# Kernel optimization log

Hardware: AMD Instinct MI355X
Metric: run time of the kernel (lower is better)

The kernel has to match this reference:

```python
import jax, jax.numpy as jnp
import numpy as np

B, LQ, LK, D, H = 4, 1024, 1024, 512, 8
HD = D // H
NEG_SLOPE = 0.2


def setup_inputs() -> dict:
    key = jax.random.key(0)
    k1, k2, k3, k4, k5 = jax.random.split(key, 5)
    query = jax.random.normal(k1, (B, LQ, D), dtype=jnp.float32)
    key_t = jax.random.normal(k2, (B, LK, D), dtype=jnp.float32)
    value = jax.random.normal(k3, (B, LK, D), dtype=jnp.float32)
    mask = jnp.ones((B, LQ, LK), dtype=jnp.int32)
    # xavier-uniform-like init for params
    limW = float(np.sqrt(6.0 / (D + D)))
    W = jax.random.uniform(k4, (D, D), minval=-limW, maxval=limW, dtype=jnp.float32)
    lima = float(np.sqrt(6.0 / (H + 2 * HD)))
    a = jax.random.uniform(k5, (1, H, 2 * HD), minval=-lima, maxval=lima, dtype=jnp.float32)
    return {"query": query, "key": key_t, "value": value, "mask": mask, "W": W, "a": a}


def reference(query, key, value, mask, W, a):
    b, lq, d = query.shape
    lk = key.shape[1]
    h = a.shape[1]
    hd = a.shape[2] // 2
    # shared linear projection (nn.Linear: x @ W.T)
    Q = (query @ W.T).reshape(b, lq, h, hd)
    K = (key @ W.T).reshape(b, lk, h, hd)
    V = (value @ W.T).reshape(b, lk, h, hd)
    # a^T [Q || K] = a_q . Q + a_k . K  (avoids the (b,lq,lk,h,2hd) concat)
    a_q = a[0, :, :hd]  # (h, hd)
    a_k = a[0, :, hd:]
    sq = jnp.einsum('bqhd,hd->bhq', Q, a_q)
    sk = jnp.einsum('bkhd,hd->bhk', K, a_k)
    scores = sq[:, :, :, None] + sk[:, :, None, :]  # (b, h, lq, lk)
    scores = jnp.where(scores >= 0, scores, NEG_SLOPE * scores)  # LeakyReLU
    scores = jnp.where(mask[:, None, :, :] == 0, -jnp.inf, scores)
    attn = jax.nn.softmax(scores, axis=-1)
    attn = jnp.where(jnp.isnan(attn), 0.0, attn)  # fully-masked rows -> 0
    out = jnp.einsum('bhqk,bkhd->bqhd', attn, V).reshape(b, lq, d)
    return out
```

## Files before the change

kernel.cpp:

```cpp
#include <hip/hip_runtime.h>
#include <hip/hip_bf16.h>

#define NEG_SLOPE 0.2f

constexpr int B = 4, LQ = 1024, LK = 1024, D = 512, H = 8, HD = 64;

typedef __attribute__((ext_vector_type(8))) short bf16x8;
typedef __attribute__((ext_vector_type(4))) float f32x4;

static __device__ __forceinline__ ushort f2bf(float x) {
  return __builtin_bit_cast(ushort, __float2bfloat16(x));
}
static __device__ __forceinline__ float bf2f(ushort u) {
  return __bfloat162float(__builtin_bit_cast(__hip_bfloat16, u));
}

__global__ void prep_wqwk(const float* __restrict__ W, const float* __restrict__ a,
                          float* __restrict__ wq, float* __restrict__ wk) {
  int tid = blockIdx.x * blockDim.x + threadIdx.x;
  int h = tid >> 9, j = tid & 511;
  const float* aq = a + h * 2 * HD;
  const float* ak = aq + HD;
  float accq = 0.f, acck = 0.f;
#pragma unroll 8
  for (int d = 0; d < HD; ++d) {
    float w = W[(size_t)(h * HD + d) * D + j];
    accq = fmaf(aq[d], w, accq);
    acck = fmaf(ak[d], w, acck);
  }
  wq[tid] = accq;
  wk[tid] = acck;
}

__global__ __launch_bounds__(256) void sqsk_kernel(
    const float* __restrict__ query, const float* __restrict__ key,
    const float* __restrict__ wq, const float* __restrict__ wk,
    float* __restrict__ sq, float* __restrict__ sk) {
  int gw = (blockIdx.x * blockDim.x + threadIdx.x) >> 6;
  int lane = threadIdx.x & 63;
  bool isK = gw >= B * LQ;
  int row = isK ? gw - B * LQ : gw;
  const float* x = (isK ? key : query) + (size_t)row * D + lane * 8;
  const float* wbase = isK ? wk : wq;
  float4 x0 = *(const float4*)x;
  float4 x1 = *(const float4*)(x + 4);
  float acc[H];
#pragma unroll
  for (int h = 0; h < H; ++h) {
    const float* w = wbase + h * D + lane * 8;
    float4 w0 = *(const float4*)w;
    float4 w1 = *(const float4*)(w + 4);
    acc[h] = x0.x * w0.x + x0.y * w0.y + x0.z * w0.z + x0.w * w0.w +
             x1.x * w1.x + x1.y * w1.y + x1.z * w1.z + x1.w * w1.w;
  }
#pragma unroll
  for (int off = 32; off > 0; off >>= 1) {
#pragma unroll
    for (int h = 0; h < H; ++h) acc[h] += __shfl_xor(acc[h], off, 64);
  }
  if (lane == 0) {
    int b = row >> 10, pos = row & 1023;
    float* dst = isK ? sk : sq;
#pragma unroll
    for (int h = 0; h < H; ++h) dst[((size_t)(b * H + h) << 10) + pos] = acc[h];
  }
}

__global__ __launch_bounds__(256) void cvt_split(
    const float* __restrict__ value, const float* __restrict__ W,
    ushort* __restrict__ val_hi, ushort* __restrict__ val_lo,
    ushort* __restrict__ w_hi, ushort* __restrict__ w_lo) {
  constexpr int VAL4 = B * LK * D / 4;
  constexpr int W4 = D * D / 4;
  int idx = blockIdx.x * 256 + threadIdx.x;
  if (idx >= VAL4 + W4) return;
  const float* src;
  ushort *dhi, *dlo;
  int off;
  if (idx < VAL4) { src = value; dhi = val_hi; dlo = val_lo; off = idx; }
  else           { src = W;     dhi = w_hi;   dlo = w_lo;   off = idx - VAL4; }
  float4 x = ((const float4*)src)[off];
  float xs[4] = {x.x, x.y, x.z, x.w};
  ushort hs[4], ls[4];
#pragma unroll
  for (int i = 0; i < 4; ++i) {
    hs[i] = f2bf(xs[i]);
    ls[i] = f2bf(xs[i] - bf2f(hs[i]));
  }
  ((ushort4*)dhi)[off] = make_ushort4(hs[0], hs[1], hs[2], hs[3]);
  ((ushort4*)dlo)[off] = make_ushort4(ls[0], ls[1], ls[2], ls[3]);
}

__global__ __launch_bounds__(256) void maskbits_kernel(const int* __restrict__ mask,
                                                       unsigned int* __restrict__ mbits) {
  int gw = (blockIdx.x * 256 + threadIdx.x) >> 6;
  int lane = threadIdx.x & 63;
#pragma unroll 4
  for (int it = 0; it < 64; ++it) {
    int wv = gw + it * 1024;
    int mv = mask[(size_t)wv * 64 + lane];
    unsigned long long bal = __ballot(mv != 0);
    if (lane == 0) *(unsigned long long*)&mbits[wv * 2] = bal;
  }
}

__global__ __launch_bounds__(256) void vproj_mfma(
    const ushort* __restrict__ val_hi, const ushort* __restrict__ val_lo,
    const ushort* __restrict__ w_hi, const ushort* __restrict__ w_lo,
    ushort* __restrict__ vt_hi, ushort* __restrict__ vt_lo) {
  __shared__ ushort as_hi[64][40], as_lo[64][40], bs_hi[64][40], bs_lo[64][40];
  int r0 = blockIdx.x * 64, c0 = blockIdx.y * 64;
  int tid = threadIdx.x, w = tid >> 6, lane = tid & 63;
  int wr = w >> 1, wc = w & 1;
  int ln15 = lane & 15, kg = lane >> 4;
  f32x4 acc[2][2] = {};
  int srow = tid >> 2, sch = (tid & 3) * 8;
  for (int k0 = 0; k0 < D; k0 += 32) {
    __syncthreads();
    *(float4*)&as_hi[srow][sch] = *(const float4*)&val_hi[(size_t)(r0 + srow) * D + k0 + sch];
    *(float4*)&as_lo[srow][sch] = *(const float4*)&val_lo[(size_t)(r0 + srow) * D + k0 + sch];
    *(float4*)&bs_hi[srow][sch] = *(const float4*)&w_hi[(size_t)(c0 + srow) * D + k0 + sch];
    *(float4*)&bs_lo[srow][sch] = *(const float4*)&w_lo[(size_t)(c0 + srow) * D + k0 + sch];
    __syncthreads();
    bf16x8 ah[2], al[2], bh[2], bl[2];
#pragma unroll
    for (int f = 0; f < 2; ++f) {
      int ra = wr * 32 + f * 16 + ln15;
      ah[f] = *(const bf16x8*)&as_hi[ra][kg * 8];
      al[f] = *(const bf16x8*)&as_lo[ra][kg * 8];
      int rb = wc * 32 + f * 16 + ln15;
      bh[f] = *(const bf16x8*)&bs_hi[rb][kg * 8];
      bl[f] = *(const bf16x8*)&bs_lo[rb][kg * 8];
    }
#pragma unroll
    for (int fm = 0; fm < 2; ++fm)
#pragma unroll
      for (int fn = 0; fn < 2; ++fn) {
        acc[fm][fn] = __builtin_amdgcn_mfma_f32_16x16x32_bf16(ah[fm], bh[fn], acc[fm][fn], 0, 0, 0);
        acc[fm][fn] = __builtin_amdgcn_mfma_f32_16x16x32_bf16(al[fm], bh[fn], acc[fm][fn], 0, 0, 0);
        acc[fm][fn] = __builtin_amdgcn_mfma_f32_16x16x32_bf16(ah[fm], bl[fn], acc[fm][fn], 0, 0, 0);
      }
  }
#pragma unroll
  for (int fm = 0; fm < 2; ++fm)
#pragma unroll
    for (int fn = 0; fn < 2; ++fn) {
      int rrow = r0 + wr * 32 + fm * 16 + (lane >> 4) * 4;
      int col = c0 + wc * 32 + fn * 16 + ln15;
      int b = rrow >> 10, k = rrow & 1023;
      int h = col >> 6, dd = col & 63;
      size_t base = ((size_t)((b * H + h) * HD + dd) << 10) + k;
      ushort hv[4], lv[4];
#pragma unroll
      for (int r = 0; r < 4; ++r) {
        float v = acc[fm][fn][r];
        hv[r] = f2bf(v);
        lv[r] = f2bf(v - bf2f(hv[r]));
      }
      *(ushort4*)&vt_hi[base] = make_ushort4(hv[0], hv[1], hv[2], hv[3]);
      *(ushort4*)&vt_lo[base] = make_ushort4(lv[0], lv[1], lv[2], lv[3]);
    }
}

__global__ __launch_bounds__(256) void attn_mfma(
    const float* __restrict__ sq, const float* __restrict__ sk,
    const unsigned int* __restrict__ mbits,
    const ushort* __restrict__ vt_hi, const ushort* __restrict__ vt_lo,
    float* __restrict__ out) {
  __shared__ float sks[LK];
  __shared__ ushort vhs[64][136], vls[64][136];
  __shared__ float linv_s[4][16];
  int bh = blockIdx.x, b = bh >> 3, h = bh & 7;
  int q0 = blockIdx.y * 64;
  int tid = threadIdx.x, w = tid >> 6, lane = tid & 63;
  int ln15 = lane & 15, kg = lane >> 4;
  int qs = q0 + w * 16 + ln15;
#pragma unroll
  for (int i = 0; i < 4; ++i) sks[i * 256 + tid] = sk[((size_t)bh << 10) + i * 256 + tid];
  float sqv = sq[((size_t)bh << 10) + qs];
  const unsigned int* mrow = mbits + ((size_t)(b << 10) + qs) * (LK / 32);
  const ushort* vhbase = vt_hi + (((size_t)bh * HD) << 10);
  const ushort* vlbase = vt_lo + (((size_t)bh * HD) << 10);
  f32x4 acc[4] = {};
  float lsum = 0.f;
  for (int tile = 0; tile < 8; ++tile) {
    int k0 = tile * 128;
    __syncthreads();
#pragma unroll
    for (int c = 0; c < 4; ++c) {
      int id = c * 256 + tid;
      int d = id >> 4, ch = id & 15;
      *(float4*)&vhs[d][ch * 8] = *(const float4*)&vhbase[((size_t)d << 10) + k0 + ch * 8];
      *(float4*)&vls[d][ch * 8] = *(const float4*)&vlbase[((size_t)d << 10) + k0 + ch * 8];
    }
    __syncthreads();
#pragma unroll
    for (int ks = 0; ks < 4; ++ks) {
      int kb = k0 + ks * 32;
      unsigned int wb = mrow[kb >> 5];
      float skv[8];
      *(float4*)&skv[0] = *(const float4*)&sks[kb + kg * 8];
      *(float4*)&skv[4] = *(const float4*)&sks[kb + kg * 8 + 4];
      bf16x8 phi, plo;
#pragma unroll
      for (int i = 0; i < 8; ++i) {
        float s = sqv + skv[i];
        float f = fmaxf(s, NEG_SLOPE * s);
        float p = ((wb >> (kg * 8 + i)) & 1u) ? __expf(f - 8.0f) : 0.f;
        lsum += p;
        ushort hb = f2bf(p);
        phi[i] = (short)hb;
        plo[i] = (short)f2bf(p - bf2f(hb));
      }
#pragma unroll
      for (int df = 0; df < 4; ++df) {
        int drow = df * 16 + ln15;
        bf16x8 bhv = *(const bf16x8*)&vhs[drow][ks * 32 + kg * 8];
        bf16x8 blv = *(const bf16x8*)&vls[drow][ks * 32 + kg * 8];
        acc[df] = __builtin_amdgcn_mfma_f32_16x16x32_bf16(phi, bhv, acc[df], 0, 0, 0);
        acc[df] = __builtin_amdgcn_mfma_f32_16x16x32_bf16(plo, bhv, acc[df], 0, 0, 0);
        acc[df] = __builtin_amdgcn_mfma_f32_16x16x32_bf16(phi, blv, acc[df], 0, 0, 0);
      }
    }
  }
  lsum += __shfl_xor(lsum, 16, 64);
  lsum += __shfl_xor(lsum, 32, 64);
  if (lane < 16) linv_s[w][ln15] = (lsum > 0.f) ? 1.f / lsum : 0.f;
  __syncthreads();
#pragma unroll
  for (int df = 0; df < 4; ++df) {
#pragma unroll
    for (int r = 0; r < 4; ++r) {
      int qrow = q0 + w * 16 + (lane >> 4) * 4 + r;
      float inv = linv_s[w][(lane >> 4) * 4 + r];
      int col = h * HD + df * 16 + ln15;
      out[((size_t)(b << 10) + qrow) * D + col] = acc[df][r] * inv;
    }
  }
}

extern "C" void kernel_launch(void* const* d_in, const int* in_sizes, int n_in,
                              void* d_out, int out_size, void* d_ws, size_t ws_size,
                              hipStream_t stream) {
  const float* query = (const float*)d_in[0];
  const float* key   = (const float*)d_in[1];
  const float* value = (const float*)d_in[2];
  const int*   mask  = (const int*)d_in[3];
  const float* W     = (const float*)d_in[4];
  const float* a     = (const float*)d_in[5];
  float* out = (float*)d_out;

  char* ws = (char*)d_ws;
  float* wq = (float*)ws;                    ws += 4096 * 4;
  float* wk = (float*)ws;                    ws += 4096 * 4;
  float* sq = (float*)ws;                    ws += 32768 * 4;
  float* sk = (float*)ws;                    ws += 32768 * 4;
  ushort* val_hi = (ushort*)ws;              ws += (size_t)B * LK * D * 2;
  ushort* val_lo = (ushort*)ws;              ws += (size_t)B * LK * D * 2;
  ushort* w_hi = (ushort*)ws;                ws += (size_t)D * D * 2;
  ushort* w_lo = (ushort*)ws;                ws += (size_t)D * D * 2;
  ushort* vt_hi = (ushort*)ws;               ws += (size_t)B * H * HD * LK * 2;
  ushort* vt_lo = (ushort*)ws;               ws += (size_t)B * H * HD * LK * 2;
  unsigned int* mbits = (unsigned int*)ws;   ws += (size_t)B * LQ * LK / 32 * 4;

  prep_wqwk<<<dim3(16), dim3(256), 0, stream>>>(W, a, wq, wk);
  cvt_split<<<dim3((B * LK * D / 4 + D * D / 4 + 255) / 256), dim3(256), 0, stream>>>(
      value, W, val_hi, val_lo, w_hi, w_lo);
  maskbits_kernel<<<dim3(256), dim3(256), 0, stream>>>(mask, mbits);
  sqsk_kernel<<<dim3(2 * B * LQ / 4), dim3(256), 0, stream>>>(query, key, wq, wk, sq, sk);
  vproj_mfma<<<dim3(B * LK / 64, D / 64), dim3(256), 0, stream>>>(
      val_hi, val_lo, w_hi, w_lo, vt_hi, vt_lo);
  attn_mfma<<<dim3(B * H, LQ / 64), dim3(256), 0, stream>>>(
      sq, sk, mbits, vt_hi, vt_lo, out);
}
```

Measured before the change: 156.3 us.

## Fuse auxiliary prep kernels and restructure projection and attention with split-K reduction

Merges the bf16 split conversion, mask bit-packing and score-vector kernels into one launch, cutting per-kernel launch and tail overhead. The V projection now loads operands directly from global memory with a 4-way split-K across waves and reduces partial sums through shared memory. The attention kernel uses 32-query tiles with a 2-way split over keys, a block order chosen so that blocks landing on the same XCD share a (batch, head), and direct global loads of V instead of LDS staging. The aim is more blocks and better occupancy, in exchange for extra shared-memory reductions and uncoalesced, unshared global loads.

```diff
diff --git a/kernel.cpp b/kernel.cpp
--- a/kernel.cpp
+++ b/kernel.cpp
@@ -32,75 +32,73 @@
   wk[tid] = acck;
 }
 
-__global__ __launch_bounds__(256) void sqsk_kernel(
+__global__ __launch_bounds__(256) void fused_aux(
     const float* __restrict__ query, const float* __restrict__ key,
+    const float* __restrict__ value, const int* __restrict__ mask,
+    const float* __restrict__ W,
     const float* __restrict__ wq, const float* __restrict__ wk,
+    ushort* __restrict__ val_hi, ushort* __restrict__ val_lo,
+    ushort* __restrict__ w_hi, ushort* __restrict__ w_lo,
+    unsigned int* __restrict__ mbits,
     float* __restrict__ sq, float* __restrict__ sk) {
-  int gw = (blockIdx.x * blockDim.x + threadIdx.x) >> 6;
-  int lane = threadIdx.x & 63;
-  bool isK = gw >= B * LQ;
-  int row = isK ? gw - B * LQ : gw;
-  const float* x = (isK ? key : query) + (size_t)row * D + lane * 8;
-  const float* wbase = isK ? wk : wq;
-  float4 x0 = *(const float4*)x;
-  float4 x1 = *(const float4*)(x + 4);
-  float acc[H];
-#pragma unroll
-  for (int h = 0; h < H; ++h) {
-    const float* w = wbase + h * D + lane * 8;
-    float4 w0 = *(const float4*)w;
-    float4 w1 = *(const float4*)(w + 4);
-    acc[h] = x0.x * w0.x + x0.y * w0.y + x0.z * w0.z + x0.w * w0.w +
-             x1.x * w1.x + x1.y * w1.y + x1.z * w1.z + x1.w * w1.w;
-  }
-#pragma unroll
-  for (int off = 32; off > 0; off >>= 1) {
-#pragma unroll
-    for (int h = 0; h < H; ++h) acc[h] += __shfl_xor(acc[h], off, 64);
-  }
-  if (lane == 0) {
-    int b = row >> 10, pos = row & 1023;
-    float* dst = isK ? sk : sq;
-#pragma unroll
-    for (int h = 0; h < H; ++h) dst[((size_t)(b * H + h) << 10) + pos] = acc[h];
-  }
-}
-
-__global__ __launch_bounds__(256) void cvt_split(
-    const float* __restrict__ value, const float* __restrict__ W,
-    ushort* __restrict__ val_hi, ushort* __restrict__ val_lo,
-    ushort* __restrict__ w_hi, ushort* __restrict__ w_lo) {
-  constexpr int VAL4 = B * LK * D / 4;
-  constexpr int W4 = D * D / 4;
-  int idx = blockIdx.x * 256 + threadIdx.x;
-  if (idx >= VAL4 + W4) return;
-  const float* src;
-  ushort *dhi, *dlo;
-  int off;
-  if (idx < VAL4) { src = value; dhi = val_hi; dlo = val_lo; off = idx; }
-  else           { src = W;     dhi = w_hi;   dlo = w_lo;   off = idx - VAL4; }
-  float4 x = ((const float4*)src)[off];
-  float xs[4] = {x.x, x.y, x.z, x.w};
-  ushort hs[4], ls[4];
-#pragma unroll
-  for (int i = 0; i < 4; ++i) {
-    hs[i] = f2bf(xs[i]);
-    ls[i] = f2bf(xs[i] - bf2f(hs[i]));
-  }
-  ((ushort4*)dhi)[off] = make_ushort4(hs[0], hs[1], hs[2], hs[3]);
-  ((ushort4*)dlo)[off] = make_ushort4(ls[0], ls[1], ls[2], ls[3]);
-}
-
-__global__ __launch_bounds__(256) void maskbits_kernel(const int* __restrict__ mask,
-                                                       unsigned int* __restrict__ mbits) {
-  int gw = (blockIdx.x * 256 + threadIdx.x) >> 6;
-  int lane = threadIdx.x & 63;
-#pragma unroll 4
-  for (int it = 0; it < 64; ++it) {
-    int wv = gw + it * 1024;
-    int mv = mask[(size_t)wv * 64 + lane];
-    unsigned long long bal = __ballot(mv != 0);
-    if (lane == 0) *(unsigned long long*)&mbits[wv * 2] = bal;
+  int blk = blockIdx.x, tid = threadIdx.x;
+  if (blk < 2304) {
+    constexpr int VAL4 = B * LK * D / 4;
+    int idx = blk * 256 + tid;
+    const float* src;
+    ushort *dhi, *dlo;
+    int off;
+    if (idx < VAL4) { src = value; dhi = val_hi; dlo = val_lo; off = idx; }
+    else           { src = W;     dhi = w_hi;   dlo = w_lo;   off = idx - VAL4; }
+    float4 x = ((const float4*)src)[off];
+    float xs[4] = {x.x, x.y, x.z, x.w};
+    ushort hs[4], ls[4];
+#pragma unroll
+    for (int i = 0; i < 4; ++i) {
+      hs[i] = f2bf(xs[i]);
+      ls[i] = f2bf(xs[i] - bf2f(hs[i]));
+    }
+    ((ushort4*)dhi)[off] = make_ushort4(hs[0], hs[1], hs[2], hs[3]);
+    ((ushort4*)dlo)[off] = make_ushort4(ls[0], ls[1], ls[2], ls[3]);
+  } else if (blk < 4352) {
+    int gw = ((blk - 2304) * 256 + tid) >> 6;
+    int lane = tid & 63;
+#pragma unroll
+    for (int it = 0; it < 8; ++it) {
+      int wv = gw * 8 + it;
+      int mv = mask[(size_t)wv * 64 + lane];
+      unsigned long long bal = __ballot(mv != 0);
+      if (lane == 0) *(unsigned long long*)&mbits[wv * 2] = bal;
+    }
+  } else {
+    int gw = ((blk - 4352) * 256 + tid) >> 6;
+    int lane = tid & 63;
+    bool isK = gw >= B * LQ;
+    int row = isK ? gw - B * LQ : gw;
+    const float* x = (isK ? key : query) + (size_t)row * D + lane * 8;
+    const float* wbase = isK ? wk : wq;
+    float4 x0 = *(const float4*)x;
+    float4 x1 = *(const float4*)(x + 4);
+    float acc[H];
+#pragma unroll
+    for (int h = 0; h < H; ++h) {
+      const float* w = wbase + h * D + lane * 8;
+      float4 w0 = *(const float4*)w;
+      float4 w1 = *(const float4*)(w + 4);
+      acc[h] = x0.x * w0.x + x0.y * w0.y + x0.z * w0.z + x0.w * w0.w +
+               x1.x * w1.x + x1.y * w1.y + x1.z * w1.z + x1.w * w1.w;
+    }
+#pragma unroll
+    for (int off = 32; off > 0; off >>= 1) {
+#pragma unroll
+      for (int h = 0; h < H; ++h) acc[h] += __shfl_xor(acc[h], off, 64);
+    }
+    if (lane == 0) {
+      int b = row >> 10, pos = row & 1023;
+      float* dst = isK ? sk : sq;
+#pragma unroll
+      for (int h = 0; h < H; ++h) dst[((size_t)(b * H + h) << 10) + pos] = acc[h];
+    }
   }
 }
 
@@ -108,32 +106,28 @@
     const ushort* __restrict__ val_hi, const ushort* __restrict__ val_lo,
     const ushort* __restrict__ w_hi, const ushort* __restrict__ w_lo,
     ushort* __restrict__ vt_hi, ushort* __restrict__ vt_lo) {
-  __shared__ ushort as_hi[64][40], as_lo[64][40], bs_hi[64][40], bs_lo[64][40];
-  int r0 = blockIdx.x * 64, c0 = blockIdx.y * 64;
+  __shared__ float vred[3][64][36];
+  int c0 = blockIdx.x * 32, r0 = blockIdx.y * 64;
   int tid = threadIdx.x, w = tid >> 6, lane = tid & 63;
-  int wr = w >> 1, wc = w & 1;
   int ln15 = lane & 15, kg = lane >> 4;
-  f32x4 acc[2][2] = {};
-  int srow = tid >> 2, sch = (tid & 3) * 8;
-  for (int k0 = 0; k0 < D; k0 += 32) {
-    __syncthreads();
-    *(float4*)&as_hi[srow][sch] = *(const float4*)&val_hi[(size_t)(r0 + srow) * D + k0 + sch];
-    *(float4*)&as_lo[srow][sch] = *(const float4*)&val_lo[(size_t)(r0 + srow) * D + k0 + sch];
-    *(float4*)&bs_hi[srow][sch] = *(const float4*)&w_hi[(size_t)(c0 + srow) * D + k0 + sch];
-    *(float4*)&bs_lo[srow][sch] = *(const float4*)&w_lo[(size_t)(c0 + srow) * D + k0 + sch];
-    __syncthreads();
-    bf16x8 ah[2], al[2], bh[2], bl[2];
-#pragma unroll
-    for (int f = 0; f < 2; ++f) {
-      int ra = wr * 32 + f * 16 + ln15;
-      ah[f] = *(const bf16x8*)&as_hi[ra][kg * 8];
-      al[f] = *(const bf16x8*)&as_lo[ra][kg * 8];
-      int rb = wc * 32 + f * 16 + ln15;
-      bh[f] = *(const bf16x8*)&bs_hi[rb][kg * 8];
-      bl[f] = *(const bf16x8*)&bs_lo[rb][kg * 8];
-    }
-#pragma unroll
-    for (int fm = 0; fm < 2; ++fm)
+  f32x4 acc[4][2] = {};
+  for (int step = 0; step < 4; ++step) {
+    int kq = w * 128 + step * 32 + kg * 8;
+    bf16x8 ah[4], al[4], bh[2], bl[2];
+#pragma unroll
+    for (int fm = 0; fm < 4; ++fm) {
+      size_t off = (size_t)(r0 + fm * 16 + ln15) * D + kq;
+      ah[fm] = *(const bf16x8*)&val_hi[off];
+      al[fm] = *(const bf16x8*)&val_lo[off];
+    }
+#pragma unroll
+    for (int fn = 0; fn < 2; ++fn) {
+      size_t off = (size_t)(c0 + fn * 16 + ln15) * D + kq;
+      bh[fn] = *(const bf16x8*)&w_hi[off];
+      bl[fn] = *(const bf16x8*)&w_lo[off];
+    }
+#pragma unroll
+    for (int fm = 0; fm < 4; ++fm)
 #pragma unroll
       for (int fn = 0; fn < 2; ++fn) {
         acc[fm][fn] = __builtin_amdgcn_mfma_f32_16x16x32_bf16(ah[fm], bh[fn], acc[fm][fn], 0, 0, 0);
@@ -141,25 +135,38 @@
         acc[fm][fn] = __builtin_amdgcn_mfma_f32_16x16x32_bf16(ah[fm], bl[fn], acc[fm][fn], 0, 0, 0);
       }
   }
-#pragma unroll
-  for (int fm = 0; fm < 2; ++fm)
-#pragma unroll
-    for (int fn = 0; fn < 2; ++fn) {
-      int rrow = r0 + wr * 32 + fm * 16 + (lane >> 4) * 4;
-      int col = c0 + wc * 32 + fn * 16 + ln15;
-      int b = rrow >> 10, k = rrow & 1023;
-      int h = col >> 6, dd = col & 63;
-      size_t base = ((size_t)((b * H + h) * HD + dd) << 10) + k;
-      ushort hv[4], lv[4];
-#pragma unroll
-      for (int r = 0; r < 4; ++r) {
-        float v = acc[fm][fn][r];
-        hv[r] = f2bf(v);
-        lv[r] = f2bf(v - bf2f(hv[r]));
-      }
-      *(ushort4*)&vt_hi[base] = make_ushort4(hv[0], hv[1], hv[2], hv[3]);
-      *(ushort4*)&vt_lo[base] = make_ushort4(lv[0], lv[1], lv[2], lv[3]);
-    }
+  if (w > 0) {
+#pragma unroll
+    for (int fm = 0; fm < 4; ++fm)
+#pragma unroll
+      for (int fn = 0; fn < 2; ++fn)
+        *(f32x4*)&vred[w - 1][lane][(fm * 2 + fn) * 4] = acc[fm][fn];
+  }
+  __syncthreads();
+  if (w == 0) {
+#pragma unroll
+    for (int fm = 0; fm < 4; ++fm)
+#pragma unroll
+      for (int fn = 0; fn < 2; ++fn) {
+#pragma unroll
+        for (int k = 0; k < 3; ++k)
+          acc[fm][fn] += *(const f32x4*)&vred[k][lane][(fm * 2 + fn) * 4];
+        int rrow = r0 + fm * 16 + (lane >> 4) * 4;
+        int col = c0 + fn * 16 + ln15;
+        int bb = rrow >> 10, kk = rrow & 1023;
+        int hh = col >> 6, dd = col & 63;
+        size_t base = ((size_t)((bb * H + hh) * HD + dd) << 10) + kk;
+        ushort hv[4], lv[4];
+#pragma unroll
+        for (int r = 0; r < 4; ++r) {
+          float v = acc[fm][fn][r];
+          hv[r] = f2bf(v);
+          lv[r] = f2bf(v - bf2f(hv[r]));
+        }
+        *(ushort4*)&vt_hi[base] = make_ushort4(hv[0], hv[1], hv[2], hv[3]);
+        *(ushort4*)&vt_lo[base] = make_ushort4(lv[0], lv[1], lv[2], lv[3]);
+      }
+  }
 }
 
 __global__ __launch_bounds__(256) void attn_mfma(
@@ -168,36 +175,40 @@
     const ushort* __restrict__ vt_hi, const ushort* __restrict__ vt_lo,
     float* __restrict__ out) {
   __shared__ float sks[LK];
-  __shared__ ushort vhs[64][136], vls[64][136];
-  __shared__ float linv_s[4][16];
-  int bh = blockIdx.x, b = bh >> 3, h = bh & 7;
-  int q0 = blockIdx.y * 64;
+  __shared__ float ared[2][64][36];
+  __shared__ float lred[2][16];
+  __shared__ float linv_s[2][16];
+  int bid = blockIdx.x;
+  int xcd = bid & 7, slot = bid >> 3;
+  int bh = xcd * 4 + (slot & 3), qt = slot >> 2;
+  int b = bh >> 3, h = bh & 7;
+  int q0 = qt * 32;
   int tid = threadIdx.x, w = tid >> 6, lane = tid & 63;
+  int strip = w & 1, khalf = w >> 1;
   int ln15 = lane & 15, kg = lane >> 4;
-  int qs = q0 + w * 16 + ln15;
+  int qs = q0 + strip * 16 + ln15;
 #pragma unroll
   for (int i = 0; i < 4; ++i) sks[i * 256 + tid] = sk[((size_t)bh << 10) + i * 256 + tid];
   float sqv = sq[((size_t)bh << 10) + qs];
   const unsigned int* mrow = mbits + ((size_t)(b << 10) + qs) * (LK / 32);
   const ushort* vhbase = vt_hi + (((size_t)bh * HD) << 10);
   const ushort* vlbase = vt_lo + (((size_t)bh * HD) << 10);
+  __syncthreads();
   f32x4 acc[4] = {};
   float lsum = 0.f;
-  for (int tile = 0; tile < 8; ++tile) {
-    int k0 = tile * 128;
-    __syncthreads();
-#pragma unroll
-    for (int c = 0; c < 4; ++c) {
-      int id = c * 256 + tid;
-      int d = id >> 4, ch = id & 15;
-      *(float4*)&vhs[d][ch * 8] = *(const float4*)&vhbase[((size_t)d << 10) + k0 + ch * 8];
-      *(float4*)&vls[d][ch * 8] = *(const float4*)&vlbase[((size_t)d << 10) + k0 + ch * 8];
-    }
-    __syncthreads();
+  for (int tile = 0; tile < 4; ++tile) {
+    int kt0 = khalf * 512 + tile * 128;
 #pragma unroll
     for (int ks = 0; ks < 4; ++ks) {
-      int kb = k0 + ks * 32;
+      int kb = kt0 + ks * 32;
       unsigned int wb = mrow[kb >> 5];
+      bf16x8 bhv[4], blv[4];
+#pragma unroll
+      for (int df = 0; df < 4; ++df) {
+        size_t off = ((size_t)(df * 16 + ln15) << 10) + kb + kg * 8;
+        bhv[df] = *(const bf16x8*)&vhbase[off];
+        blv[df] = *(const bf16x8*)&vlbase[off];
+      }
       float skv[8];
       *(float4*)&skv[0] = *(const float4*)&sks[kb + kg * 8];
       *(float4*)&skv[4] = *(const float4*)&sks[kb + kg * 8 + 4];
@@ -214,27 +225,37 @@
       }
 #pragma unroll
       for (int df = 0; df < 4; ++df) {
-        int drow = df * 16 + ln15;
-        bf16x8 bhv = *(const bf16x8*)&vhs[drow][ks * 32 + kg * 8];
-        bf16x8 blv = *(const bf16x8*)&vls[drow][ks * 32 + kg * 8];
-        acc[df] = __builtin_amdgcn_mfma_f32_16x16x32_bf16(phi, bhv, acc[df], 0, 0, 0);
-        acc[df] = __builtin_amdgcn_mfma_f32_16x16x32_bf16(plo, bhv, acc[df], 0, 0, 0);
-        acc[df] = __builtin_amdgcn_mfma_f32_16x16x32_bf16(phi, blv, acc[df], 0, 0, 0);
+        acc[df] = __builtin_amdgcn_mfma_f32_16x16x32_bf16(phi, bhv[df], acc[df], 0, 0, 0);
+        acc[df] = __builtin_amdgcn_mfma_f32_16x16x32_bf16(plo, bhv[df], acc[df], 0, 0, 0);
+        acc[df] = __builtin_amdgcn_mfma_f32_16x16x32_bf16(phi, blv[df], acc[df], 0, 0, 0);
       }
     }
   }
   lsum += __shfl_xor(lsum, 16, 64);
   lsum += __shfl_xor(lsum, 32, 64);
-  if (lane < 16) linv_s[w][ln15] = (lsum > 0.f) ? 1.f / lsum : 0.f;
+  if (khalf == 1) {
+#pragma unroll
+    for (int df = 0; df < 4; ++df)
+      *(f32x4*)&ared[strip][lane][df * 4] = acc[df];
+    if (lane < 16) lred[strip][lane] = lsum;
+  }
   __syncthreads();
-#pragma unroll
-  for (int df = 0; df < 4; ++df) {
-#pragma unroll
-    for (int r = 0; r < 4; ++r) {
-      int qrow = q0 + w * 16 + (lane >> 4) * 4 + r;
-      float inv = linv_s[w][(lane >> 4) * 4 + r];
-      int col = h * HD + df * 16 + ln15;
-      out[((size_t)(b << 10) + qrow) * D + col] = acc[df][r] * inv;
+  if (khalf == 0) {
+#pragma unroll
+    for (int df = 0; df < 4; ++df)
+      acc[df] += *(const f32x4*)&ared[strip][lane][df * 4];
+    lsum += lred[strip][ln15];
+    if (lane < 16) linv_s[strip][lane] = (lsum > 0.f) ? 1.f / lsum : 0.f;
+#pragma unroll
+    for (int df = 0; df < 4; ++df) {
+#pragma unroll
+      for (int r = 0; r < 4; ++r) {
+        int crow = (lane >> 4) * 4 + r;
+        int qrow = q0 + strip * 16 + crow;
+        float inv = linv_s[strip][crow];
+        int col = h * HD + df * 16 + ln15;
+        out[((size_t)(b << 10) + qrow) * D + col] = acc[df][r] * inv;
+      }
     }
   }
 }
@@ -264,12 +285,11 @@
   unsigned int* mbits = (unsigned int*)ws;   ws += (size_t)B * LQ * LK / 32 * 4;
 
   prep_wqwk<<<dim3(16), dim3(256), 0, stream>>>(W, a, wq, wk);
-  cvt_split<<<dim3((B * LK * D / 4 + D * D / 4 + 255) / 256), dim3(256), 0, stream>>>(
-      value, W, val_hi, val_lo, w_hi, w_lo);
-  maskbits_kernel<<<dim3(256), dim3(256), 0, stream>>>(mask, mbits);
-  sqsk_kernel<<<dim3(2 * B * LQ / 4), dim3(256), 0, stream>>>(query, key, wq, wk, sq, sk);
-  vproj_mfma<<<dim3(B * LK / 64, D / 64), dim3(256), 0, stream>>>(
+  fused_aux<<<dim3(6400), dim3(256), 0, stream>>>(
+      query, key, value, mask, W, wq, wk,
+      val_hi, val_lo, w_hi, w_lo, mbits, sq, sk);
+  vproj_mfma<<<dim3(D / 32, B * LK / 64), dim3(256), 0, stream>>>(
       val_hi, val_lo, w_hi, w_lo, vt_hi, vt_lo);
-  attn_mfma<<<dim3(B * H, LQ / 64), dim3(256), 0, stream>>>(
+  attn_mfma<<<dim3(32 * LQ / 32), dim3(256), 0, stream>>>(
       sq, sk, mbits, vt_hi, vt_lo, out);
 }
```

Measured after the change: 184.9 us. 1.18x slower.
